# Optimization experiments

Measured on AMD Instinct MI355X. Metric: run time of the kernel, lower is better.

Reference implementation:

```python
import jax, jax.numpy as jnp
import numpy as np

VOCAB, EMBED, HIDDEN = 10000, 256, 512


def setup_inputs() -> dict:
    key = jax.random.key(0)
    ks = jax.random.split(key, 16)
    u = lambda k, shape, fan: jax.random.uniform(k, shape, jnp.float32) * np.sqrt(2.0 / fan)
    inp = {
        "input_": jax.random.randint(ks[0], (128, 64), 0, VOCAB, dtype=jnp.int64) if jax.config.jax_enable_x64 else jax.random.randint(ks[0], (128, 64), 0, VOCAB, dtype=jnp.int32),
        "embeddings": jax.random.normal(ks[1], (VOCAB, EMBED), jnp.float32),
        "W_xi": u(ks[2], (EMBED, HIDDEN), EMBED + HIDDEN),
        "W_hi": u(ks[3], (HIDDEN, HIDDEN), 2 * HIDDEN),
        "b_i": jax.random.uniform(ks[4], (1, HIDDEN), jnp.float32),
        "W_xf": u(ks[5], (EMBED, HIDDEN), EMBED + HIDDEN),
        "W_hf": u(ks[6], (HIDDEN, HIDDEN), 2 * HIDDEN),
        "b_f": jax.random.uniform(ks[7], (1, HIDDEN), jnp.float32),
        "W_xc": u(ks[8], (EMBED, HIDDEN), EMBED + HIDDEN),
        "W_hc": u(ks[9], (HIDDEN, HIDDEN), 2 * HIDDEN),
        "b_c": jax.random.uniform(ks[10], (1, HIDDEN), jnp.float32),
        "W_xo": u(ks[11], (EMBED, HIDDEN), EMBED + HIDDEN),
        "W_ho": u(ks[12], (HIDDEN, HIDDEN), 2 * HIDDEN),
        "b_o": jax.random.uniform(ks[13], (1, HIDDEN), jnp.float32),
        "W": u(ks[14], (HIDDEN, VOCAB), HIDDEN + VOCAB),
        "b": jax.random.uniform(ks[15], (1, VOCAB), jnp.float32),
    }
    return inp


def reference(input_, embeddings, W_xi, W_hi, b_i, W_xf, W_hf, b_f,
              W_xc, W_hc, b_c, W_xo, W_ho, b_o, W, b):
    T, B = input_.shape
    H = W_hi.shape[0]
    embeds = embeddings[input_]  # [T, B, E]
    # Precompute input-to-gate projections for all timesteps (batched GEMMs)
    xi = jnp.einsum('tbe,eh->tbh', embeds, W_xi) + b_i
    xf = jnp.einsum('tbe,eh->tbh', embeds, W_xf) + b_f
    xc = jnp.einsum('tbe,eh->tbh', embeds, W_xc) + b_c
    xo = jnp.einsum('tbe,eh->tbh', embeds, W_xo) + b_o

    def step(carry, xs):
        h_t, c_t = carry
        xi_t, xf_t, xc_t, xo_t = xs
        i_t = jax.nn.sigmoid(xi_t + h_t @ W_hi)
        f_t = jax.nn.sigmoid(xf_t + h_t @ W_hf)
        g_t = jnp.tanh(xc_t + h_t @ W_hc)
        o_t = jax.nn.sigmoid(xo_t + h_t @ W_ho)
        c_t = f_t * c_t + i_t * g_t
        h_t = o_t * jnp.tanh(c_t)
        return (h_t, c_t), h_t

    h0 = jnp.zeros((B, H), jnp.float32)
    c0 = jnp.zeros((B, H), jnp.float32)
    (h_t, c_t), hs = jax.lax.scan(step, (h0, c0), (xi, xf, xc, xo))  # hs: [T, B, H]
    # Output projection batched over all timesteps, matching torch.cat(tmp, 0)
    output = hs.reshape(T * B, H) @ W + b  # [T*B, VOCAB]
    return output, (h_t, c_t)
```

## Files before the change

### kernel.cpp

```cpp
#include <hip/hip_runtime.h>
#include <stdint.h>

#define T_STEPS 128
#define BATCH   64
#define EMBED   256
#define HIDDEN  512
#define VOCAB   10000
#define M_ROWS  (T_STEPS*BATCH)
#define NGATE   (4*HIDDEN)
#define NBLK    32
#define NLAUNCH 256
#define NGEMM   (NLAUNCH-NBLK)
#define NTILE_N 125
#define NTILE_M 64

typedef __attribute__((ext_vector_type(2))) float  f32x2;
typedef __attribute__((ext_vector_type(4))) float  f32x4;
typedef __attribute__((ext_vector_type(4))) int    i32x4;
typedef __attribute__((ext_vector_type(8))) __bf16 bf16x8;

static __device__ __forceinline__ unsigned short f32_to_bf16(float f) {
    union { float f; uint32_t u; } v; v.f = f;
    uint32_t u = v.u;
    return (unsigned short)((u + 0x7FFFu + ((u >> 16) & 1u)) >> 16);
}
static __device__ __forceinline__ float sigf(float x) {
    return 1.f / (1.f + __expf(-x));
}
static __device__ __forceinline__ float tanhfast(float x) {
    float e = __expf(2.f * fminf(fmaxf(x, -15.f), 15.f));
    return (e - 1.f) / (e + 1.f);
}
static __device__ __forceinline__ void cell2(
    float pi0, float pi1, float pf0, float pf1, float pg0, float pg1,
    float po0, float po1, float& c0, float& c1, float& h0, float& h1) {
    float i0 = sigf(pi0), i1 = sigf(pi1);
    float f0 = sigf(pf0), f1 = sigf(pf1);
    float g0 = tanhfast(pg0), g1 = tanhfast(pg1);
    float o0 = sigf(po0), o1 = sigf(po1);
    c0 = f0 * c0 + i0 * g0;
    c1 = f1 * c1 + i1 * g1;
    h0 = o0 * tanhfast(c0);
    h1 = o1 * tanhfast(c1);
}

static __device__ __forceinline__ i32x4 ld16ic(const void* p) {
    i32x4 r; asm volatile("global_load_dwordx4 %0, %1, off sc0 sc1" : "=v"(r) : "v"(p)); return r;
}
static __device__ __forceinline__ unsigned ld4ic(const void* p) {
    unsigned r; asm volatile("global_load_dword %0, %1, off sc0 sc1" : "=v"(r) : "v"(p)); return r;
}
static __device__ __forceinline__ void st4ic(void* p, unsigned v) {
    asm volatile("global_store_dword %0, %1, off sc0 sc1" :: "v"(p), "v"(v) : "memory");
}

__global__ void poison_hsbf(unsigned* __restrict__ hs, unsigned* __restrict__ fl) {
    size_t i = (size_t)blockIdx.x * 256 + threadIdx.x;
    if (i < 524288) {
        i32x4 v = { -1, -1, -1, -1 };
        asm volatile("global_store_dwordx4 %0, %1, off sc0 sc1"
                     :: "v"((char*)hs + i * 16), "v"(v) : "memory");
    } else if (i < 524288 + 2048) {
        i32x4 z = { 0, 0, 0, 0 };
        asm volatile("global_store_dwordx4 %0, %1, off sc0 sc1"
                     :: "v"((char*)fl + (i - 524288) * 16), "v"(z) : "memory");
    }
}

__global__ void wt_convert(const float* __restrict__ W, unsigned short* __restrict__ Wt) {
    __shared__ float tile[32][33];
    int n0 = blockIdx.x * 32;
    int k0 = blockIdx.y * 32;
    int tx = threadIdx.x, ty = threadIdx.y;
    int n = n0 + tx;
    if (n < VOCAB) tile[ty][tx] = W[(size_t)(k0 + ty) * VOCAB + n];
    __syncthreads();
    int nn = n0 + ty;
    if (nn < VOCAB) Wt[(size_t)nn * HIDDEN + k0 + tx] = f32_to_bf16(tile[tx][ty]);
}

__global__ void wh_convert(const float* __restrict__ Whi, const float* __restrict__ Whf,
                           const float* __restrict__ Whc, const float* __restrict__ Who,
                           unsigned short* __restrict__ WhT) {
    __shared__ float tile[32][33];
    int g = blockIdx.z;
    const float* Wg = (g == 0) ? Whi : (g == 1) ? Whf : (g == 2) ? Whc : Who;
    int n0 = blockIdx.x * 32, k0 = blockIdx.y * 32;
    int tx = threadIdx.x, ty = threadIdx.y;
    tile[ty][tx] = Wg[(size_t)(k0 + ty) * HIDDEN + n0 + tx];
    __syncthreads();
    WhT[((size_t)g * HIDDEN + n0 + ty) * HIDDEN + k0 + tx] = f32_to_bf16(tile[tx][ty]);
}

__global__ void emb_convert(const float* __restrict__ E, unsigned short* __restrict__ Eb) {
    size_t i = ((size_t)blockIdx.x * 256 + threadIdx.x) * 4;
    if (i >= (size_t)VOCAB * EMBED) return;
    f32x4 v = *reinterpret_cast<const f32x4*>(E + i);
    unsigned short o[4];
    #pragma unroll
    for (int j = 0; j < 4; ++j) o[j] = f32_to_bf16(v[j]);
    *reinterpret_cast<unsigned long long*>(Eb + i) =
        ((unsigned long long)o[3] << 48) | ((unsigned long long)o[2] << 32) |
        ((unsigned long long)o[1] << 16) | (unsigned long long)o[0];
}

__global__ void wx_convert(const float* __restrict__ Wxi, const float* __restrict__ Wxf,
                           const float* __restrict__ Wxc, const float* __restrict__ Wxo,
                           unsigned short* __restrict__ WxT) {
    __shared__ float tile[32][33];
    int g = blockIdx.z;
    const float* Wg = (g == 0) ? Wxi : (g == 1) ? Wxf : (g == 2) ? Wxc : Wxo;
    int n0 = blockIdx.x * 32, k0 = blockIdx.y * 32;
    int tx = threadIdx.x, ty = threadIdx.y;
    tile[ty][tx] = Wg[(size_t)(k0 + ty) * HIDDEN + n0 + tx];
    __syncthreads();
    WxT[((size_t)g * HIDDEN + n0 + ty) * EMBED + k0 + tx] = f32_to_bf16(tile[tx][ty]);
}

__global__ __launch_bounds__(256) void xproj_mfma(
    const int* __restrict__ idx, const unsigned short* __restrict__ Eb,
    const unsigned short* __restrict__ WxT,
    const float* __restrict__ bi,  const float* __restrict__ bf_,
    const float* __restrict__ bc,  const float* __restrict__ bo,
    float* __restrict__ xg)
{
    __shared__ __align__(16) char sA[128 * 128];
    __shared__ __align__(16) char sB[64 * 128];
    int n0 = blockIdx.x * 64;
    int m0 = blockIdx.y * 128;
    int tid = threadIdx.x;
    int w = tid >> 6, lane = tid & 63;
    f32x4 acc[2][4] = {};

    int arow[4], aer[4];
    #pragma unroll
    for (int i = 0; i < 4; ++i) {
        int s = tid + i * 256;
        arow[i] = s >> 3;
        aer[i]  = idx[m0 + arow[i]];
    }

    for (int kc = 0; kc < 4; ++kc) {
        int k0 = kc * 64;
        #pragma unroll
        for (int i = 0; i < 4; ++i) {
            int s = tid + i * 256;
            int row = arow[i], slot = s & 7;
            i32x4 v = *reinterpret_cast<const i32x4*>(Eb + (size_t)aer[i] * EMBED + k0 + slot * 8);
            *reinterpret_cast<i32x4*>(sA + row * 128 + ((slot ^ (row & 7)) * 16)) = v;
        }
        #pragma unroll
        for (int i = 0; i < 2; ++i) {
            int s = tid + i * 256;
            int row = s >> 3, slot = s & 7;
            i32x4 v = *reinterpret_cast<const i32x4*>(WxT + (size_t)(n0 + row) * EMBED + k0 + slot * 8);
            *reinterpret_cast<i32x4*>(sB + row * 128 + ((slot ^ (row & 7)) * 16)) = v;
        }
        __syncthreads();
        #pragma unroll
        for (int k2 = 0; k2 < 2; ++k2) {
            bf16x8 a[2], b[4];
            #pragma unroll
            for (int rf = 0; rf < 2; ++rf) {
                int row = w * 32 + rf * 16 + (lane & 15);
                int off = (k2 * 64 + (lane >> 4) * 16) ^ ((row & 7) << 4);
                a[rf] = *reinterpret_cast<const bf16x8*>(sA + row * 128 + off);
            }
            #pragma unroll
            for (int cf = 0; cf < 4; ++cf) {
                int row = cf * 16 + (lane & 15);
                int off = (k2 * 64 + (lane >> 4) * 16) ^ ((row & 7) << 4);
                b[cf] = *reinterpret_cast<const bf16x8*>(sB + row * 128 + off);
            }
            #pragma unroll
            for (int rf = 0; rf < 2; ++rf)
                #pragma unroll
                for (int cf = 0; cf < 4; ++cf)
                    acc[rf][cf] = __builtin_amdgcn_mfma_f32_16x16x32_bf16(a[rf], b[cf], acc[rf][cf], 0, 0, 0);
        }
        __syncthreads();
    }
    #pragma unroll
    for (int cf = 0; cf < 4; ++cf) {
        int col = n0 + cf * 16 + (lane & 15);
        int g = col >> 9, hc = col & 511;
        const float* bg = (g == 0) ? bi : (g == 1) ? bf_ : (g == 2) ? bc : bo;
        float bv = bg[hc];
        #pragma unroll
        for (int rf = 0; rf < 2; ++rf)
            #pragma unroll
            for (int r = 0; r < 4; ++r) {
                int row = m0 + w * 32 + rf * 16 + (lane >> 4) * 4 + r;
                xg[(size_t)row * NGATE + col] = acc[rf][cf][r] + bv;
            }
    }
}

__global__ __launch_bounds__(512) void lstm_fused(
    const float* __restrict__ xg,
    const unsigned short* __restrict__ WhT,
    unsigned short* hsbf,
    float* __restrict__ hfin, float* __restrict__ cfin,
    const unsigned short* __restrict__ Btbf,
    const float* __restrict__ bias,
    float* __restrict__ Cout,
    unsigned* flags)
{
    __shared__ __align__(16) unsigned char smem[41472];
    const int tid = threadIdx.x;

    if (blockIdx.x < NBLK) {
        unsigned char* hstage = smem;
        auto P_lds = reinterpret_cast<float (*)[32][17]>(smem + 32768);
        const int bx   = blockIdx.x;
        const int hc0  = bx * 16;
        const int lane = tid & 63, w = tid >> 6;
        const int wm   = w >> 2, wg = w & 3;

        bf16x8 breg[16];
        {
            const unsigned short* base =
                WhT + ((size_t)wg * HIDDEN + hc0 + (lane & 15)) * HIDDEN + (lane >> 4) * 8;
            #pragma unroll
            for (int ks = 0; ks < 16; ++ks)
                breg[ks] = *reinterpret_cast<const bf16x8*>(base + ks * 32);
        }

        const int ub  = tid >> 3;
        const int uhp = tid & 7;
        const int uhc = hc0 + uhp * 2;
        float cA0 = 0.f, cA1 = 0.f, cB0 = 0.f, cB1 = 0.f;
        f32x2 xvA[4], xvB[4];
        if (tid < 256) {
            const float* xrA = xg + (size_t)(0 * 32 + ub) * NGATE + uhc;
            const float* xrB = xg + (size_t)(1 * 32 + ub) * NGATE + uhc;
            #pragma unroll
            for (int g = 0; g < 4; ++g) {
                xvA[g] = *reinterpret_cast<const f32x2*>(xrA + g * HIDDEN);
                xvB[g] = *reinterpret_cast<const f32x2*>(xrB + g * HIDDEN);
            }
        }
        unsigned* hs32 = reinterpret_cast<unsigned*>(hsbf);

#define CHK(R) { mx = (mx > (unsigned)R[0]) ? mx : (unsigned)R[0]; \
                 mx = (mx > (unsigned)R[1]) ? mx : (unsigned)R[1]; \
                 mx = (mx > (unsigned)R[2]) ? mx : (unsigned)R[2]; \
                 mx = (mx > (unsigned)R[3]) ? mx : (unsigned)R[3]; }
#define STLDS(R, I) { int s16 = (I) * 512 + tid; int row = s16 >> 6, sl = s16 & 63; \
        *reinterpret_cast<i32x4*>(hstage + row * 1024 + ((sl ^ (row & 7)) << 4)) = R; }

#define GROUP_UPDATE(G, XV, C0, C1, TT)                                         \
    if (tid < 256) {                                                            \
        int hp2 = uhp * 2;                                                      \
        float h0, h1;                                                           \
        cell2(P_lds[0][ub][hp2] + XV[0][0], P_lds[0][ub][hp2+1] + XV[0][1],     \
              P_lds[1][ub][hp2] + XV[1][0], P_lds[1][ub][hp2+1] + XV[1][1],     \
              P_lds[2][ub][hp2] + XV[2][0], P_lds[2][ub][hp2+1] + XV[2][1],     \
              P_lds[3][ub][hp2] + XV[3][0], P_lds[3][ub][hp2+1] + XV[3][1],     \
              C0, C1, h0, h1);                                                  \
        unsigned hp = ((unsigned)f32_to_bf16(h1) << 16) | (unsigned)f32_to_bf16(h0); \
        st4ic(hs32 + (size_t)(TT) * 16384 + ((G) * 32 + ub) * 256 + (uhc >> 1), hp); \
        if ((TT) == T_STEPS - 1) {                                              \
            f32x2 hv = { h0, h1 };                                              \
            *reinterpret_cast<f32x2*>(hfin + (size_t)((G) * 32 + ub) * HIDDEN + uhc) = hv; \
            f32x2 cv = { C0, C1 };                                              \
            *reinterpret_cast<f32x2*>(cfin + (size_t)((G) * 32 + ub) * HIDDEN + uhc) = cv; \
        } else {                                                                \
            const float* xr = xg + (size_t)(((TT) + 1) * BATCH + (G) * 32 + ub) * NGATE + uhc; \
            _Pragma("unroll")                                                   \
            for (int g = 0; g < 4; ++g)                                         \
                XV[g] = *reinterpret_cast<const f32x2*>(xr + g * HIDDEN);       \
        }                                                                       \
    }

#define GROUP_PHASE(G, XV, C0, C1, TT)                                          \
    {                                                                           \
        f32x4 acc = {0.f, 0.f, 0.f, 0.f};                                       \
        {                                                                       \
            const char* hb = (const char*)hsbf + (size_t)((TT) - 1) * 65536 + (G) * 32768; \
            i32x4 q0, q1, q2, q3;                                               \
            for (int rnd = 0; rnd < (1 << 16); ++rnd) {                         \
                q0 = ld16ic(hb + (size_t)(0 * 512 + tid) * 16);                 \
                q1 = ld16ic(hb + (size_t)(1 * 512 + tid) * 16);                 \
                q2 = ld16ic(hb + (size_t)(2 * 512 + tid) * 16);                 \
                q3 = ld16ic(hb + (size_t)(3 * 512 + tid) * 16);                 \
                asm volatile("s_waitcnt vmcnt(0)"                               \
                    : "+v"(q0), "+v"(q1), "+v"(q2), "+v"(q3));                  \
                unsigned mx = 0u;                                               \
                CHK(q0) CHK(q1) CHK(q2) CHK(q3)                                 \
                if (mx != 0xFFFFFFFFu) break;                                   \
                __builtin_amdgcn_s_sleep(1);                                    \
            }                                                                   \
            __builtin_amdgcn_sched_barrier(0);                                  \
            STLDS(q0, 0) STLDS(q1, 1) STLDS(q2, 2) STLDS(q3, 3)                 \
        }                                                                       \
        __syncthreads();     \
        if (tid == 0) {                                                         \
            int s_ = 2 * (TT) + (G);                                            \
            int ps = s_ - 1;                                                    \
            st4ic(flags + ((size_t)(ps >> 1) * 64 + (ps & 1) * 32 + bx), 1u);   \
            if (s_ == 2) st4ic(flags + bx, 1u);             \
        }                                                                       \
        {                                                                       \
            const int rr = wm * 16 + (lane & 15);                               \
            _Pragma("unroll")                                                   \
            for (int ks = 0; ks < 16; ++ks) {                                   \
                int sl = ks * 4 + (lane >> 4);                                  \
                bf16x8 a = *reinterpret_cast<const bf16x8*>(                    \
                    hstage + rr * 1024 + ((sl ^ (rr & 7)) << 4));               \
                acc = __builtin_amdgcn_mfma_f32_16x16x32_bf16(a, breg[ks], acc, 0, 0, 0); \
            }                                                                   \
        }                                                                       \
        {                                                                       \
            int colr = lane & 15, rowb = (lane >> 4) * 4;                       \
            _Pragma("unroll")                                                   \
            for (int r = 0; r < 4; ++r)                                         \
                P_lds[wg][wm * 16 + rowb + r][colr] = acc[r];                   \
        }                                                                       \
        __syncthreads();                                                        \
        GROUP_UPDATE(G, XV, C0, C1, TT)                                         \
    }

        if (tid < 256) {
            float h0, h1;
            cell2(xvA[0][0], xvA[0][1], xvA[1][0], xvA[1][1],
                  xvA[2][0], xvA[2][1], xvA[3][0], xvA[3][1], cA0, cA1, h0, h1);
            unsigned hp = ((unsigned)f32_to_bf16(h1) << 16) | (unsigned)f32_to_bf16(h0);
            st4ic(hs32 + (size_t)(0 * 32 + ub) * 256 + (uhc >> 1), hp);
            const float* xr = xg + (size_t)(1 * BATCH + 0 * 32 + ub) * NGATE + uhc;
            #pragma unroll
            for (int g = 0; g < 4; ++g)
                xvA[g] = *reinterpret_cast<const f32x2*>(xr + g * HIDDEN);

            cell2(xvB[0][0], xvB[0][1], xvB[1][0], xvB[1][1],
                  xvB[2][0], xvB[2][1], xvB[3][0], xvB[3][1], cB0, cB1, h0, h1);
            hp = ((unsigned)f32_to_bf16(h1) << 16) | (unsigned)f32_to_bf16(h0);
            st4ic(hs32 + (size_t)(1 * 32 + ub) * 256 + (uhc >> 1), hp);
            xr = xg + (size_t)(1 * BATCH + 1 * 32 + ub) * NGATE + uhc;
            #pragma unroll
            for (int g = 0; g < 4; ++g)
                xvB[g] = *reinterpret_cast<const f32x2*>(xr + g * HIDDEN);
        }

        for (int t = 1; t < T_STEPS; ++t) {
            GROUP_PHASE(0, xvA, cA0, cA1, t)
            GROUP_PHASE(1, xvB, cB0, cB1, t)
        }
#undef GROUP_PHASE
#undef GROUP_UPDATE
#undef STLDS
#undef CHK
        __syncthreads();
        if (tid == 0)
            st4ic(flags + ((size_t)127 * 64 + 32 + bx), 1u);
    } else {
        char* sA = (char*)smem;
        char* sB = (char*)smem + 16384;
        const int gbid = blockIdx.x - NBLK;
        const int w = tid >> 6, lane = tid & 63;
        const unsigned short* __restrict__ Abf = hsbf;

        int ni, mi_lo, mi_hi;
        if (gbid < 99)       { ni = gbid;       mi_lo = 0;  mi_hi = 32; }
        else if (gbid < 125) { ni = gbid;       mi_lo = 0;  mi_hi = 64; }
        else                 { ni = gbid - 125; mi_lo = 32; mi_hi = 64; }
        const int n0 = ni * 80;

        for (int mi = mi_lo; mi < mi_hi; ++mi) {
            int m0 = mi * 128;
            {
                const unsigned* fl = flags + (size_t)2 * mi * 64;
                for (int rnd = 0; rnd < (1 << 20); ++rnd) {
                    unsigned v = 1u;
                    if (tid < 128) v = ld4ic(fl + tid);
                    asm volatile("s_waitcnt vmcnt(0)" : "+v"(v));
                    int bad = (tid < 128) && (v == 0u);
                    if (__syncthreads_count(bad) == 0) break;
                    __builtin_amdgcn_s_sleep(16);
                }
                asm volatile("" ::: "memory");
            }
            f32x4 acc[5] = {};
            for (int kc = 0; kc < 8; ++kc) {
                int k0 = kc * 64;
                #pragma unroll
                for (int i = 0; i < 2; ++i) {
                    int s = tid + i * 512;
                    int row = s >> 3, slot = s & 7;
                    i32x4 v = *reinterpret_cast<const i32x4*>(
                        Abf + (size_t)(m0 + row) * HIDDEN + k0 + slot * 8);
                    *reinterpret_cast<i32x4*>(sA + row * 128 + ((slot ^ (row & 7)) * 16)) = v;
                }
                {
                    int s = tid, br = s >> 3, bs = s & 7;
                    i32x4 v = *reinterpret_cast<const i32x4*>(
                        Btbf + (size_t)(n0 + br) * HIDDEN + k0 + bs * 8);
                    *reinterpret_cast<i32x4*>(sB + br * 128 + ((bs ^ (br & 7)) * 16)) = v;
                    if (tid < 128) {
                        s = 512 + tid; br = s >> 3; bs = s & 7;
                        v = *reinterpret_cast<const i32x4*>(
                            Btbf + (size_t)(n0 + br) * HIDDEN + k0 + bs * 8);
                        *reinterpret_cast<i32x4*>(sB + br * 128 + ((bs ^ (br & 7)) * 16)) = v;
                    }
                }
                __syncthreads();
                #pragma unroll
                for (int k2 = 0; k2 < 2; ++k2) {
                    int arow = w * 16 + (lane & 15);
                    int aoff = (k2 * 64 + (lane >> 4) * 16) ^ ((arow & 7) << 4);
                    bf16x8 a = *reinterpret_cast<const bf16x8*>(sA + arow * 128 + aoff);
                    #pragma unroll
                    for (int cf = 0; cf < 5; ++cf) {
                        int brow = cf * 16 + (lane & 15);
                        int boff = (k2 * 64 + (lane >> 4) * 16) ^ ((brow & 7) << 4);
                        bf16x8 b = *reinterpret_cast<const bf16x8*>(sB + brow * 128 + boff);
                        acc[cf] = __builtin_amdgcn_mfma_f32_16x16x32_bf16(a, b, acc[cf], 0, 0, 0);
                    }
                }
                __syncthreads();
            }
            #pragma unroll
            for (int cf = 0; cf < 5; ++cf) {
                int col = n0 + cf * 16 + (lane & 15);
                float bv = bias[col];
                #pragma unroll
                for (int r = 0; r < 4; ++r) {
                    int row = m0 + w * 16 + (lane >> 4) * 4 + r;
                    Cout[(size_t)row * VOCAB + col] = acc[cf][r] + bv;
                }
            }
        }
    }
}

__global__ void finalize_hc(const float* __restrict__ hfin, const float* __restrict__ cfin,
                            float* __restrict__ out) {
    int i = blockIdx.x * 256 + threadIdx.x;
    size_t base = (size_t)M_ROWS * VOCAB;
    if (i < BATCH * HIDDEN)
        out[base + i] = hfin[i];
    else
        out[base + i] = cfin[i - BATCH * HIDDEN];
}

extern "C" void kernel_launch(void* const* d_in, const int* in_sizes, int n_in,
                              void* d_out, int out_size, void* d_ws, size_t ws_size,
                              hipStream_t stream) {
    (void)in_sizes; (void)n_in; (void)out_size; (void)ws_size;
    const int*   input_ = (const int*)  d_in[0];
    const float* Emb    = (const float*)d_in[1];
    const float* Wxi    = (const float*)d_in[2];
    const float* Whi    = (const float*)d_in[3];
    const float* bi     = (const float*)d_in[4];
    const float* Wxf    = (const float*)d_in[5];
    const float* Whf    = (const float*)d_in[6];
    const float* bf_    = (const float*)d_in[7];
    const float* Wxc    = (const float*)d_in[8];
    const float* Whc    = (const float*)d_in[9];
    const float* bc     = (const float*)d_in[10];
    const float* Wxo    = (const float*)d_in[11];
    const float* Who    = (const float*)d_in[12];
    const float* bo     = (const float*)d_in[13];
    const float* W      = (const float*)d_in[14];
    const float* b      = (const float*)d_in[15];
    float* out = (float*)d_out;

    char* ws = (char*)d_ws;
    float*          xg   = (float*)         (ws);
    unsigned short* hsbf = (unsigned short*)(ws +  67108864);
    unsigned short* Wtbf = (unsigned short*)(ws +  75497472);
    unsigned short* WhT  = (unsigned short*)(ws +  85737472);
    unsigned short* Embb = (unsigned short*)(ws +  87834624);
    unsigned short* WxT  = (unsigned short*)(ws +  92954624);
    float*          hfin = (float*)         (ws +  94003200);
    float*          cbuf = (float*)         (ws +  94134272);
    unsigned*       flags= (unsigned*)      (ws +  94265344);

    poison_hsbf<<<2057, 256, 0, stream>>>((unsigned*)hsbf, flags);
    wt_convert<<<dim3(313, 16), dim3(32, 32), 0, stream>>>(W, Wtbf);
    wh_convert<<<dim3(16, 16, 4), dim3(32, 32), 0, stream>>>(Whi, Whf, Whc, Who, WhT);
    emb_convert<<<2500, 256, 0, stream>>>(Emb, Embb);
    wx_convert<<<dim3(16, 8, 4), dim3(32, 32), 0, stream>>>(Wxi, Wxf, Wxc, Wxo, WxT);
    xproj_mfma<<<dim3(32, 64), 256, 0, stream>>>(input_, Embb, WxT, bi, bf_, bc, bo, xg);

    {
        const float* xg_c = xg;
        const unsigned short* WhT_c = WhT;
        unsigned short* hsbf_p = hsbf;
        float* hfin_p = hfin; float* cbuf_p = cbuf;
        const unsigned short* Wtbf_c = Wtbf;
        const float* b_c = b;
        float* out_p = out;
        unsigned* flags_p = flags;
        void* args[] = { (void*)&xg_c, (void*)&WhT_c, (void*)&hsbf_p,
                         (void*)&hfin_p, (void*)&cbuf_p,
                         (void*)&Wtbf_c, (void*)&b_c, (void*)&out_p, (void*)&flags_p };
        hipLaunchCooperativeKernel((void*)lstm_fused, dim3(NLAUNCH), dim3(512), args, 0, stream);
    }

    finalize_hc<<<256, 256, 0, stream>>>(hfin, cbuf, out);
}
```

Measured before the change: 615.5 us.

## Merge prep kernels, write final h/c directly, prefetch GEMM tiles into registers

Three changes. The embedding bf16 conversion is fused with the hs poison and flag-clear kernel, and the finalize_hc kernel is removed by having the fused LSTM kernel write the final h and c straight into the output tail. Together these drop two kernel launches. The output-projection GEMM loop now register-prefetches the next K chunk of A and B while the current chunk is consumed, overlapping global loads with MFMA work at the cost of extra registers.

```diff
diff --git a/kernel.cpp b/kernel.cpp
--- a/kernel.cpp
+++ b/kernel.cpp
@@ -54,16 +54,28 @@
     asm volatile("global_store_dword %0, %1, off sc0 sc1" :: "v"(p), "v"(v) : "memory");
 }
 
-__global__ void poison_hsbf(unsigned* __restrict__ hs, unsigned* __restrict__ fl) {
-    size_t i = (size_t)blockIdx.x * 256 + threadIdx.x;
-    if (i < 524288) {
+__global__ void prep0(const float* __restrict__ E, unsigned short* __restrict__ Eb,
+                      unsigned* __restrict__ hs, unsigned* __restrict__ fl) {
+    size_t t = (size_t)blockIdx.x * 256 + threadIdx.x;
+    size_t i = t * 4;
+    if (i < (size_t)VOCAB * EMBED) {
+        f32x4 v = *reinterpret_cast<const f32x4*>(E + i);
+        unsigned short o[4];
+        #pragma unroll
+        for (int j = 0; j < 4; ++j) o[j] = f32_to_bf16(v[j]);
+        *reinterpret_cast<unsigned long long*>(Eb + i) =
+            ((unsigned long long)o[3] << 48) | ((unsigned long long)o[2] << 32) |
+            ((unsigned long long)o[1] << 16) | (unsigned long long)o[0];
+    }
+    if (t < 524288) {
         i32x4 v = { -1, -1, -1, -1 };
         asm volatile("global_store_dwordx4 %0, %1, off sc0 sc1"
-                     :: "v"((char*)hs + i * 16), "v"(v) : "memory");
-    } else if (i < 524288 + 2048) {
+                     :: "v"((char*)hs + t * 16), "v"(v) : "memory");
+    }
+    if (t < 2048) {
         i32x4 z = { 0, 0, 0, 0 };
         asm volatile("global_store_dwordx4 %0, %1, off sc0 sc1"
-                     :: "v"((char*)fl + (i - 524288) * 16), "v"(z) : "memory");
+                     :: "v"((char*)fl + t * 16), "v"(z) : "memory");
     }
 }
 
@@ -90,18 +102,6 @@
     tile[ty][tx] = Wg[(size_t)(k0 + ty) * HIDDEN + n0 + tx];
     __syncthreads();
     WhT[((size_t)g * HIDDEN + n0 + ty) * HIDDEN + k0 + tx] = f32_to_bf16(tile[tx][ty]);
-}
-
-__global__ void emb_convert(const float* __restrict__ E, unsigned short* __restrict__ Eb) {
-    size_t i = ((size_t)blockIdx.x * 256 + threadIdx.x) * 4;
-    if (i >= (size_t)VOCAB * EMBED) return;
-    f32x4 v = *reinterpret_cast<const f32x4*>(E + i);
-    unsigned short o[4];
-    #pragma unroll
-    for (int j = 0; j < 4; ++j) o[j] = f32_to_bf16(v[j]);
-    *reinterpret_cast<unsigned long long*>(Eb + i) =
-        ((unsigned long long)o[3] << 48) | ((unsigned long long)o[2] << 32) |
-        ((unsigned long long)o[1] << 16) | (unsigned long long)o[0];
 }
 
 __global__ void wx_convert(const float* __restrict__ Wxi, const float* __restrict__ Wxf,
@@ -200,7 +200,7 @@
     const float* __restrict__ xg,
     const unsigned short* __restrict__ WhT,
     unsigned short* hsbf,
-    float* __restrict__ hfin, float* __restrict__ cfin,
+    float* __restrict__ outp,
     const unsigned short* __restrict__ Btbf,
     const float* __restrict__ bias,
     float* __restrict__ Cout,
@@ -262,9 +262,9 @@
         st4ic(hs32 + (size_t)(TT) * 16384 + ((G) * 32 + ub) * 256 + (uhc >> 1), hp); \
         if ((TT) == T_STEPS - 1) {                                              \
             f32x2 hv = { h0, h1 };                                              \
-            *reinterpret_cast<f32x2*>(hfin + (size_t)((G) * 32 + ub) * HIDDEN + uhc) = hv; \
+            *reinterpret_cast<f32x2*>(outp + (size_t)((G) * 32 + ub) * HIDDEN + uhc) = hv; \
             f32x2 cv = { C0, C1 };                                              \
-            *reinterpret_cast<f32x2*>(cfin + (size_t)((G) * 32 + ub) * HIDDEN + uhc) = cv; \
+            *reinterpret_cast<f32x2*>(outp + 32768 + (size_t)((G) * 32 + ub) * HIDDEN + uhc) = cv; \
         } else {                                                                \
             const float* xr = xg + (size_t)(((TT) + 1) * BATCH + (G) * 32 + ub) * NGATE + uhc; \
             _Pragma("unroll")                                                   \
@@ -366,6 +366,10 @@
         else                 { ni = gbid - 125; mi_lo = 32; mi_hi = 64; }
         const int n0 = ni * 80;
 
+        const int ar0 = tid >> 3, ar1 = (tid >> 3) + 64, aslot = tid & 7;
+        const int br0 = tid >> 3, bs0 = tid & 7;
+        const int br1 = (512 + tid) >> 3, bs1 = tid & 7;
+
         for (int mi = mi_lo; mi < mi_hi; ++mi) {
             int m0 = mi * 128;
             {
@@ -381,29 +385,29 @@
                 asm volatile("" ::: "memory");
             }
             f32x4 acc[5] = {};
+            i32x4 ra0, ra1, rb0, rb1;
+            {
+                ra0 = *reinterpret_cast<const i32x4*>(Abf + (size_t)(m0 + ar0) * HIDDEN + aslot * 8);
+                ra1 = *reinterpret_cast<const i32x4*>(Abf + (size_t)(m0 + ar1) * HIDDEN + aslot * 8);
+                rb0 = *reinterpret_cast<const i32x4*>(Btbf + (size_t)(n0 + br0) * HIDDEN + bs0 * 8);
+                if (tid < 128)
+                    rb1 = *reinterpret_cast<const i32x4*>(Btbf + (size_t)(n0 + br1) * HIDDEN + bs1 * 8);
+            }
             for (int kc = 0; kc < 8; ++kc) {
-                int k0 = kc * 64;
-                #pragma unroll
-                for (int i = 0; i < 2; ++i) {
-                    int s = tid + i * 512;
-                    int row = s >> 3, slot = s & 7;
-                    i32x4 v = *reinterpret_cast<const i32x4*>(
-                        Abf + (size_t)(m0 + row) * HIDDEN + k0 + slot * 8);
-                    *reinterpret_cast<i32x4*>(sA + row * 128 + ((slot ^ (row & 7)) * 16)) = v;
+                *reinterpret_cast<i32x4*>(sA + ar0 * 128 + ((aslot ^ (ar0 & 7)) * 16)) = ra0;
+                *reinterpret_cast<i32x4*>(sA + ar1 * 128 + ((aslot ^ (ar1 & 7)) * 16)) = ra1;
+                *reinterpret_cast<i32x4*>(sB + br0 * 128 + ((bs0 ^ (br0 & 7)) * 16)) = rb0;
+                if (tid < 128)
+                    *reinterpret_cast<i32x4*>(sB + br1 * 128 + ((bs1 ^ (br1 & 7)) * 16)) = rb1;
+                __syncthreads();
+                if (kc < 7) {
+                    int k1 = (kc + 1) * 64;
+                    ra0 = *reinterpret_cast<const i32x4*>(Abf + (size_t)(m0 + ar0) * HIDDEN + k1 + aslot * 8);
+                    ra1 = *reinterpret_cast<const i32x4*>(Abf + (size_t)(m0 + ar1) * HIDDEN + k1 + aslot * 8);
+                    rb0 = *reinterpret_cast<const i32x4*>(Btbf + (size_t)(n0 + br0) * HIDDEN + k1 + bs0 * 8);
+                    if (tid < 128)
+                        rb1 = *reinterpret_cast<const i32x4*>(Btbf + (size_t)(n0 + br1) * HIDDEN + k1 + bs1 * 8);
                 }
-                {
-                    int s = tid, br = s >> 3, bs = s & 7;
-                    i32x4 v = *reinterpret_cast<const i32x4*>(
-                        Btbf + (size_t)(n0 + br) * HIDDEN + k0 + bs * 8);
-                    *reinterpret_cast<i32x4*>(sB + br * 128 + ((bs ^ (br & 7)) * 16)) = v;
-                    if (tid < 128) {
-                        s = 512 + tid; br = s >> 3; bs = s & 7;
-                        v = *reinterpret_cast<const i32x4*>(
-                            Btbf + (size_t)(n0 + br) * HIDDEN + k0 + bs * 8);
-                        *reinterpret_cast<i32x4*>(sB + br * 128 + ((bs ^ (br & 7)) * 16)) = v;
-                    }
-                }
-                __syncthreads();
                 #pragma unroll
                 for (int k2 = 0; k2 < 2; ++k2) {
                     int arow = w * 16 + (lane & 15);
@@ -431,16 +435,6 @@
             }
         }
     }
-}
-
-__global__ void finalize_hc(const float* __restrict__ hfin, const float* __restrict__ cfin,
-                            float* __restrict__ out) {
-    int i = blockIdx.x * 256 + threadIdx.x;
-    size_t base = (size_t)M_ROWS * VOCAB;
-    if (i < BATCH * HIDDEN)
-        out[base + i] = hfin[i];
-    else
-        out[base + i] = cfin[i - BATCH * HIDDEN];
 }
 
 extern "C" void kernel_launch(void* const* d_in, const int* in_sizes, int n_in,
@@ -472,14 +466,11 @@
     unsigned short* WhT  = (unsigned short*)(ws +  85737472);
     unsigned short* Embb = (unsigned short*)(ws +  87834624);
     unsigned short* WxT  = (unsigned short*)(ws +  92954624);
-    float*          hfin = (float*)         (ws +  94003200);
-    float*          cbuf = (float*)         (ws +  94134272);
-    unsigned*       flags= (unsigned*)      (ws +  94265344);
-
-    poison_hsbf<<<2057, 256, 0, stream>>>((unsigned*)hsbf, flags);
+    unsigned*       flags= (unsigned*)      (ws +  94003200);
+
+    prep0<<<2500, 256, 0, stream>>>(Emb, Embb, (unsigned*)hsbf, flags);
     wt_convert<<<dim3(313, 16), dim3(32, 32), 0, stream>>>(W, Wtbf);
     wh_convert<<<dim3(16, 16, 4), dim3(32, 32), 0, stream>>>(Whi, Whf, Whc, Who, WhT);
-    emb_convert<<<2500, 256, 0, stream>>>(Emb, Embb);
     wx_convert<<<dim3(16, 8, 4), dim3(32, 32), 0, stream>>>(Wxi, Wxf, Wxc, Wxo, WxT);
     xproj_mfma<<<dim3(32, 64), 256, 0, stream>>>(input_, Embb, WxT, bi, bf_, bc, bo, xg);
 
@@ -487,16 +478,14 @@
         const float* xg_c = xg;
         const unsigned short* WhT_c = WhT;
         unsigned short* hsbf_p = hsbf;
-        float* hfin_p = hfin; float* cbuf_p = cbuf;
+        float* outp = out + (size_t)M_ROWS * VOCAB;
         const unsigned short* Wtbf_c = Wtbf;
         const float* b_c = b;
         float* out_p = out;
         unsigned* flags_p = flags;
         void* args[] = { (void*)&xg_c, (void*)&WhT_c, (void*)&hsbf_p,
-                         (void*)&hfin_p, (void*)&cbuf_p,
+                         (void*)&outp,
                          (void*)&Wtbf_c, (void*)&b_c, (void*)&out_p, (void*)&flags_p };
         hipLaunchCooperativeKernel((void*)lstm_fused, dim3(NLAUNCH), dim3(512), args, 0, stream);
     }
-
-    finalize_hc<<<256, 256, 0, stream>>>(hfin, cbuf, out);
-}
+}
```

Measured after the change: 600.8 us. 1.02x faster.
